# Performance work log

Measured on AMD Instinct MI355X. Metric: run time of the kernel, lower is better.

## Reference

```python
import jax, jax.numpy as jnp
import numpy as np

S = 64.0
M = 0.5
EPS = 1e-07
NORM_EPS = 1e-12  # matches torch F.normalize default eps
B, D, C = 512, 512, 64000


def _l2_normalize(a, axis=-1):
    n = jnp.sqrt(jnp.sum(a * a, axis=axis, keepdims=True))
    return a / jnp.maximum(n, NORM_EPS)


def setup_inputs() -> dict:
    key = jax.random.key(0)
    kx, ky, kw = jax.random.split(key, 3)
    x = jax.random.normal(kx, (B, D), dtype=jnp.float32)
    y = jax.random.randint(ky, (B,), 0, C, dtype=jnp.int64)
    # kaiming_uniform-ish init: bound = sqrt(6 / fan_in)
    bound = np.sqrt(6.0 / D).astype(np.float32)
    W = jax.random.uniform(kw, (C, D), dtype=jnp.float32, minval=-bound, maxval=bound)
    return {"x": x, "y": y, "W": W}


def reference(x, y, W):
    # cosine similarities: [B, C]
    theta = _l2_normalize(x) @ _l2_normalize(W).T
    # target logit per row
    tgt = jnp.take_along_axis(theta, y[:, None], axis=1)[:, 0]  # [B]
    numerator = S * jnp.cos(jnp.arccos(jnp.clip(tgt, -1.0 + EPS, 1.0 - EPS)) + M)
    # sum of exp(s*theta) over non-target classes (mask out target column)
    is_tgt = jnp.arange(C, dtype=y.dtype)[None, :] == y[:, None]  # [B, C]
    excl_sum = jnp.sum(jnp.where(is_tgt, 0.0, jnp.exp(S * theta)), axis=1)  # [B]
    denominator = jnp.exp(numerator) + excl_sum
    return -jnp.mean(numerator - jnp.log(denominator))
```

## Files before the change

### kernel.cpp

```cpp
#include <hip/hip_runtime.h>


#define B_N 512
#define D_N 512
#define C_N 64000
#define S_SCALE 64.0f
#define MARGIN 0.5f
#define EPS_C 1e-7f
#define NREP 16

typedef unsigned short ushort_t;
typedef __attribute__((ext_vector_type(8))) short short8;
typedef __attribute__((ext_vector_type(4))) float floatx4;

__device__ __forceinline__ ushort_t f2bf(float f) {
    unsigned int u = __float_as_uint(f);
    u += 0x7fffu + ((u >> 16) & 1u);
    return (ushort_t)(u >> 16);
}

__global__ void xprep_kernel(const float* __restrict__ x,
                             ushort_t* __restrict__ xnT,
                             float* __restrict__ rowsumR) {
    int b = blockIdx.x;
    int t = threadIdx.x;
    if (b == 128) {
#pragma unroll
        for (int i = 0; i < NREP * B_N / 256; ++i)
            rowsumR[i * 256 + t] = 0.0f;
        return;
    }
    int row  = b * 4 + (t >> 6);
    int lane = t & 63;
    const float4* p = (const float4*)(x + (size_t)row * D_N);
    float4 v0 = p[lane * 2];
    float4 v1 = p[lane * 2 + 1];
    float ss = v0.x*v0.x + v0.y*v0.y + v0.z*v0.z + v0.w*v0.w
             + v1.x*v1.x + v1.y*v1.y + v1.z*v1.z + v1.w*v1.w;
#pragma unroll
    for (int off = 32; off > 0; off >>= 1) ss += __shfl_xor(ss, off);
    float sc = 1.0f / fmaxf(sqrtf(ss), 1e-12f);
    uint4 o;
    o.x = (unsigned)f2bf(v0.x*sc) | ((unsigned)f2bf(v0.y*sc) << 16);
    o.y = (unsigned)f2bf(v0.z*sc) | ((unsigned)f2bf(v0.w*sc) << 16);
    o.z = (unsigned)f2bf(v1.x*sc) | ((unsigned)f2bf(v1.y*sc) << 16);
    o.w = (unsigned)f2bf(v1.z*sc) | ((unsigned)f2bf(v1.w*sc) << 16);
    *((uint4*)(xnT + ((size_t)(lane << 9) + row) * 8)) = o;
}

__global__ __launch_bounds__(512, 4)
void gemm_fused_kernel(const float* __restrict__ W,
                       const ushort_t* __restrict__ xnT,
                       const int* __restrict__ y,
                       float* __restrict__ rowsumR,
                       float* __restrict__ tgt) {
    __shared__ ushort_t sW[64 * 512];

    int t    = threadIdx.x;
    int lane = t & 63;
    int w    = t >> 6;
    int lq   = lane >> 4;
    int lc   = lane & 15;
    int cn0  = blockIdx.x * 64;

#pragma unroll
    for (int rr = 0; rr < 8; ++rr) {
        int row = w * 8 + rr;
        const float4* p = (const float4*)(W + (size_t)(cn0 + row) * D_N);
        float4 a = p[lane * 2];
        float4 b = p[lane * 2 + 1];
        float ss = a.x*a.x + a.y*a.y + a.z*a.z + a.w*a.w
                 + b.x*b.x + b.y*b.y + b.z*b.z + b.w*b.w;
#pragma unroll
        for (int off = 32; off > 0; off >>= 1) ss += __shfl_xor(ss, off);
        float sc = 1.0f / fmaxf(sqrtf(ss), 1e-12f);
        uint4 o;
        o.x = (unsigned)f2bf(a.x*sc) | ((unsigned)f2bf(a.y*sc) << 16);
        o.y = (unsigned)f2bf(a.z*sc) | ((unsigned)f2bf(a.w*sc) << 16);
        o.z = (unsigned)f2bf(b.x*sc) | ((unsigned)f2bf(b.y*sc) << 16);
        o.w = (unsigned)f2bf(b.z*sc) | ((unsigned)f2bf(b.w*sc) << 16);
        int kc = lane;
        int rs = row ^ (kc & 7);
        *((uint4*)(sW + kc * 512 + rs * 8)) = o;
    }
    __syncthreads();

    floatx4 acc[4][4];
#pragma unroll
    for (int i = 0; i < 4; i++)
#pragma unroll
        for (int j = 0; j < 4; j++) acc[i][j] = (floatx4){0.f, 0.f, 0.f, 0.f};

    const ushort_t* apT[4];
#pragma unroll
    for (int tm = 0; tm < 4; tm++)
        apT[tm] = xnT + ((size_t)lq * 512 + w * 64 + tm * 16 + lc) * 8;

    for (int k = 0; k < 16; ++k) {
        short8 af[4], bfr[4];
#pragma unroll
        for (int tm = 0; tm < 4; tm++)
            af[tm] = *(const short8*)(apT[tm] + k * 16384);
        int kc = k * 4 + lq;
#pragma unroll
        for (int tn = 0; tn < 4; tn++) {
            int rs = (tn * 16 + lc) ^ (kc & 7);
            bfr[tn] = *(const short8*)(sW + kc * 512 + rs * 8);
        }
#pragma unroll
        for (int tm = 0; tm < 4; tm++)
#pragma unroll
            for (int tn = 0; tn < 4; tn++)
                acc[tm][tn] = __builtin_amdgcn_mfma_f32_16x16x32_bf16(
                    af[tm], bfr[tn], acc[tm][tn], 0, 0, 0);
    }

    __syncthreads();
    float* rowacc = (float*)sW;
#pragma unroll
    for (int tm = 0; tm < 4; tm++) {
#pragma unroll
        for (int r = 0; r < 4; r++) {
            int lrow = w * 64 + tm * 16 + lq * 4 + r;
            int yv   = y[lrow];
            float esum = 0.0f;
#pragma unroll
            for (int tn = 0; tn < 4; tn++) {
                int gcol = cn0 + tn * 16 + lc;
                float theta = acc[tm][tn][r];
                if (gcol == yv) {
                    tgt[lrow] = theta;
                } else {
                    esum += __expf(S_SCALE * theta);
                }
            }
#pragma unroll
            for (int off = 1; off < 16; off <<= 1) esum += __shfl_xor(esum, off);
            if (lc == 0) rowacc[lrow] = esum;
        }
    }
    __syncthreads();
    atomicAdd(&rowsumR[(blockIdx.x & (NREP - 1)) * B_N + t], rowacc[t]);
}

__global__ void finalize_kernel(const float* __restrict__ rowsumR,
                                const float* __restrict__ tgt,
                                float* __restrict__ out) {
    __shared__ float red[256];
    int t = threadIdx.x;
    float s = 0.0f;
    for (int r = t; r < B_N; r += 256) {
        float rs = 0.0f;
#pragma unroll
        for (int i = 0; i < NREP; ++i) rs += rowsumR[i * B_N + r];
        float tv = tgt[r];
        tv = fminf(fmaxf(tv, -1.0f + EPS_C), 1.0f - EPS_C);
        float num = S_SCALE * cosf(acosf(tv) + MARGIN);
        float den = expf(num) + rs;
        s += num - logf(den);
    }
    red[t] = s;
    __syncthreads();
    for (int o = 128; o > 0; o >>= 1) {
        if (t < o) red[t] += red[t + o];
        __syncthreads();
    }
    if (t == 0) out[0] = -red[0] / (float)B_N;
}

extern "C" void kernel_launch(void* const* d_in, const int* in_sizes, int n_in,
                              void* d_out, int out_size, void* d_ws, size_t ws_size,
                              hipStream_t stream) {
    const float* x = (const float*)d_in[0];
    const int*   y = (const int*)d_in[1];
    const float* W = (const float*)d_in[2];
    float* out = (float*)d_out;

    char* ws = (char*)d_ws;
    ushort_t* xnT   = (ushort_t*)ws;
    float* rowsumR  = (float*)(ws + 524288);
    float* tgt      = rowsumR + NREP * B_N;

    xprep_kernel<<<129, 256, 0, stream>>>(x, xnT, rowsumR);
    gemm_fused_kernel<<<C_N / 64, 512, 0, stream>>>(W, xnT, y, rowsumR, tgt);
    finalize_kernel<<<1, 256, 0, stream>>>(rowsumR, tgt, out);
}
```

Baseline: 226.9 us.

## Stream W tile through double-buffered LDS and defer normalization to epilogue

```diff
diff --git a/kernel.cpp b/kernel.cpp
--- a/kernel.cpp
+++ b/kernel.cpp
@@ -54,7 +54,9 @@
                        const int* __restrict__ y,
                        float* __restrict__ rowsumR,
                        float* __restrict__ tgt) {
-    __shared__ ushort_t sW[64 * 512];
+    __shared__ ushort_t bufB[2][4096];
+    __shared__ float    rnormS[64];
+    __shared__ float    rowacc[512];
 
     int t    = threadIdx.x;
     int lane = t & 63;
@@ -62,61 +64,72 @@
     int lq   = lane >> 4;
     int lc   = lane & 15;
     int cn0  = blockIdx.x * 64;
-
-#pragma unroll
-    for (int rr = 0; rr < 8; ++rr) {
-        int row = w * 8 + rr;
-        const float4* p = (const float4*)(W + (size_t)(cn0 + row) * D_N);
-        float4 a = p[lane * 2];
-        float4 b = p[lane * 2 + 1];
-        float ss = a.x*a.x + a.y*a.y + a.z*a.z + a.w*a.w
-                 + b.x*b.x + b.y*b.y + b.z*b.z + b.w*b.w;
-#pragma unroll
-        for (int off = 32; off > 0; off >>= 1) ss += __shfl_xor(ss, off);
-        float sc = 1.0f / fmaxf(sqrtf(ss), 1e-12f);
-        uint4 o;
-        o.x = (unsigned)f2bf(a.x*sc) | ((unsigned)f2bf(a.y*sc) << 16);
-        o.y = (unsigned)f2bf(a.z*sc) | ((unsigned)f2bf(a.w*sc) << 16);
-        o.z = (unsigned)f2bf(b.x*sc) | ((unsigned)f2bf(b.y*sc) << 16);
-        o.w = (unsigned)f2bf(b.z*sc) | ((unsigned)f2bf(b.w*sc) << 16);
-        int kc = lane;
-        int rs = row ^ (kc & 7);
-        *((uint4*)(sW + kc * 512 + rs * 8)) = o;
-    }
-    __syncthreads();
-
-    floatx4 acc[4][4];
-#pragma unroll
-    for (int i = 0; i < 4; i++)
-#pragma unroll
-        for (int j = 0; j < 4; j++) acc[i][j] = (floatx4){0.f, 0.f, 0.f, 0.f};
+    int col  = t >> 3;
+    int kcl  = t & 7;
+
+    const float4* gW = (const float4*)(W + (size_t)(cn0 + col) * D_N + kcl * 8);
 
     const ushort_t* apT[4];
 #pragma unroll
     for (int tm = 0; tm < 4; tm++)
         apT[tm] = xnT + ((size_t)lq * 512 + w * 64 + tm * 16 + lc) * 8;
 
-    for (int k = 0; k < 16; ++k) {
-        short8 af[4], bfr[4];
-#pragma unroll
-        for (int tm = 0; tm < 4; tm++)
-            af[tm] = *(const short8*)(apT[tm] + k * 16384);
-        int kc = k * 4 + lq;
-#pragma unroll
-        for (int tn = 0; tn < 4; tn++) {
-            int rs = (tn * 16 + lc) ^ (kc & 7);
-            bfr[tn] = *(const short8*)(sW + kc * 512 + rs * 8);
+    floatx4 acc[4][4];
+#pragma unroll
+    for (int i = 0; i < 4; i++)
+#pragma unroll
+        for (int j = 0; j < 4; j++) acc[i][j] = (floatx4){0.f, 0.f, 0.f, 0.f};
+    float ssq = 0.0f;
+
+    float4 w0 = gW[0];
+    float4 w1 = gW[1];
+
+    for (int s = 0; s < 8; ++s) {
+        int cur = s & 1;
+        ssq += w0.x*w0.x + w0.y*w0.y + w0.z*w0.z + w0.w*w0.w
+             + w1.x*w1.x + w1.y*w1.y + w1.z*w1.z + w1.w*w1.w;
+        uint4 pk;
+        pk.x = (unsigned)f2bf(w0.x) | ((unsigned)f2bf(w0.y) << 16);
+        pk.y = (unsigned)f2bf(w0.z) | ((unsigned)f2bf(w0.w) << 16);
+        pk.z = (unsigned)f2bf(w1.x) | ((unsigned)f2bf(w1.y) << 16);
+        pk.w = (unsigned)f2bf(w1.z) | ((unsigned)f2bf(w1.w) << 16);
+        *(uint4*)&bufB[cur][kcl * 512 + (col ^ kcl) * 8] = pk;
+        __syncthreads();
+
+        if (s < 7) {
+            w0 = gW[(s + 1) * 16];
+            w1 = gW[(s + 1) * 16 + 1];
         }
-#pragma unroll
-        for (int tm = 0; tm < 4; tm++)
+
+#pragma unroll
+        for (int h = 0; h < 2; ++h) {
+            short8 af[4], bfr[4];
+#pragma unroll
+            for (int tm = 0; tm < 4; tm++)
+                af[tm] = *(const short8*)(apT[tm] + (s * 2 + h) * 16384);
+            int kb = h * 4 + lq;
 #pragma unroll
             for (int tn = 0; tn < 4; tn++)
-                acc[tm][tn] = __builtin_amdgcn_mfma_f32_16x16x32_bf16(
-                    af[tm], bfr[tn], acc[tm][tn], 0, 0, 0);
-    }
-
+                bfr[tn] = *(const short8*)
+                    &bufB[cur][kb * 512 + ((tn * 16 + lc) ^ kb) * 8];
+#pragma unroll
+            for (int tm = 0; tm < 4; tm++)
+#pragma unroll
+                for (int tn = 0; tn < 4; tn++)
+                    acc[tm][tn] = __builtin_amdgcn_mfma_f32_16x16x32_bf16(
+                        af[tm], bfr[tn], acc[tm][tn], 0, 0, 0);
+        }
+        __syncthreads();
+    }
+
+#pragma unroll
+    for (int off = 1; off < 8; off <<= 1) ssq += __shfl_xor(ssq, off);
+    if (kcl == 0) rnormS[col] = 1.0f / fmaxf(sqrtf(ssq), 1e-12f);
     __syncthreads();
-    float* rowacc = (float*)sW;
+
+    float rn[4];
+#pragma unroll
+    for (int tn = 0; tn < 4; tn++) rn[tn] = rnormS[tn * 16 + lc];
 #pragma unroll
     for (int tm = 0; tm < 4; tm++) {
 #pragma unroll
@@ -127,7 +140,7 @@
 #pragma unroll
             for (int tn = 0; tn < 4; tn++) {
                 int gcol = cn0 + tn * 16 + lc;
-                float theta = acc[tm][tn][r];
+                float theta = acc[tm][tn][r] * rn[tn];
                 if (gcol == yv) {
                     tgt[lrow] = theta;
                 } else {
```

Result: slower. 254.8 us (+12.3%).
